# Optimization experiments

Measured on AMD Instinct MI355X. Metric: run time of the kernel, lower is better.

Reference implementation:

```python
import jax, jax.numpy as jnp
import numpy as np

NPG = 39      # nodes per graph, from (1+8+64+9)*(39+1)=3280 = lin1 in_features
NEG_SLOPE = 0.2


def gat_conv(x, src, dst, W, a_src, a_dst, b, n):
    """PyG GATConv, heads=1, self-loops already appended to (src, dst).
    x:[N,Fin] W:[Fin,Fout] a_src/a_dst:[Fout] b:[Fout] -> [N,Fout]"""
    h = x @ W                                        # [N,Fout]
    e = jax.nn.leaky_relu(h[src] @ a_src + h[dst] @ a_dst, NEG_SLOPE)  # [E]
    m = jax.lax.stop_gradient(jax.ops.segment_max(e, dst, num_segments=n))
    w = jnp.exp(e - m[dst])
    denom = jax.ops.segment_sum(w, dst, num_segments=n)
    alpha = w / (denom[dst] + 1e-16)                 # segment softmax per target node
    out = jax.ops.segment_sum(alpha[:, None] * h[src], dst, num_segments=n)
    return out + b


def setup_inputs() -> dict:
    key = jax.random.key(0)
    ks = jax.random.split(key, 20)
    B, DEG = 4096, 8
    N = B * NPG
    E = N * DEG
    x = jax.random.normal(ks[0], (N, 1), dtype=jnp.float32)
    # block-diagonal edges: each node emits DEG edges to random nodes in SAME graph
    src = jnp.repeat(jnp.arange(N, dtype=jnp.int64), DEG)
    offs = (src // NPG) * NPG
    dst = offs + jax.random.randint(ks[1], (E,), 0, NPG, dtype=jnp.int64)
    edge_index = jnp.stack([src, dst])
    batch_vec = jnp.repeat(jnp.arange(B, dtype=jnp.int64), NPG)

    def glorot(k, shape):
        fan = shape[0] + (shape[1] if len(shape) > 1 else 1)
        s = jnp.sqrt(6.0 / fan)
        return jax.random.uniform(k, shape, jnp.float32, -s, s)

    p = {
        'W1': glorot(ks[2], (1, 8)),   'a1s': glorot(ks[3], (8,)),  'a1d': glorot(ks[4], (8,)),  'b1': jnp.zeros((8,), jnp.float32),
        'W2': glorot(ks[5], (8, 64)),  'a2s': glorot(ks[6], (64,)), 'a2d': glorot(ks[7], (64,)), 'b2': jnp.zeros((64,), jnp.float32),
        'W3': glorot(ks[8], (64, 9)),  'a3s': glorot(ks[9], (9,)),  'a3d': glorot(ks[10], (9,)), 'b3': jnp.zeros((9,), jnp.float32),
        'lW1': glorot(ks[11], (3280, 5000)), 'lb1': jnp.zeros((5000,), jnp.float32),
        'lW2': glorot(ks[12], (5000, 1024)), 'lb2': jnp.zeros((1024,), jnp.float32),
        'lW3': glorot(ks[13], (1024, 9)),    'lb3': jnp.zeros((9,), jnp.float32),
    }
    return {'x': x, 'edge_index': edge_index, 'batch_vec': batch_vec, **p}


def reference(x, edge_index, batch_vec,
              W1, a1s, a1d, b1, W2, a2s, a2d, b2, W3, a3s, a3d, b3,
              lW1, lb1, lW2, lb2, lW3, lb3):
    N = x.shape[0]
    B = N // NPG
    loops = jnp.arange(N, dtype=edge_index.dtype)
    src = jnp.concatenate([edge_index[0], loops])   # GATConv add_self_loops=True
    dst = jnp.concatenate([edge_index[1], loops])

    res = x.reshape(B, -1)                                    # [B,39]
    out0 = jax.ops.segment_max(x, batch_vec, num_segments=B)  # [B,1]

    h1 = jax.nn.relu(gat_conv(x, src, dst, W1, a1s, a1d, b1, N))   # dropout = eval no-op
    res1 = h1.reshape(B, -1)                                   # [B,312]
    out1 = jax.ops.segment_max(h1, batch_vec, num_segments=B)

    h2 = jax.nn.relu(gat_conv(h1, src, dst, W2, a2s, a2d, b2, N))
    res2 = h2.reshape(B, -1)                                   # [B,2496]
    out2 = jax.ops.segment_max(h2, batch_vec, num_segments=B)

    h3 = jax.nn.relu(gat_conv(h2, src, dst, W3, a3s, a3d, b3, N))
    res3 = h3.reshape(B, -1)                                   # [B,351]
    out3 = jax.ops.segment_max(h3, batch_vec, num_segments=B)

    f = jnp.concatenate([res, res1, res2, res3, out0, out1, out2, out3], axis=1)  # [B,3280]
    f = jax.nn.relu(f @ lW1 + lb1)
    f = jax.nn.relu(f @ lW2 + lb2)
    return f @ lW3 + lb3                                       # [B,9]
```

## Files before the change

### kernel.cpp

```cpp
#include <hip/hip_runtime.h>
#include <hip/hip_bf16.h>
#include <hip/hip_fp16.h>
#include <stdint.h>


typedef float f32x4 __attribute__((ext_vector_type(4)));
typedef short bf16x8 __attribute__((ext_vector_type(8)));
typedef _Float16 f16x8 __attribute__((ext_vector_type(8)));

__device__ __forceinline__ unsigned fenc(float f) {
  int s = __float_as_int(f);
  return s < 0 ? ~(unsigned)s : ((unsigned)s | 0x80000000u);
}
__device__ __forceinline__ float fdec(unsigned u) {
  return (u & 0x80000000u) ? __int_as_float((int)(u & 0x7fffffffu))
                           : __int_as_float(~(int)u);
}

__device__ __forceinline__ void ldsbar() {
  asm volatile("s_waitcnt lgkmcnt(0)\n\ts_barrier" ::: "memory");
}


__global__ __launch_bounds__(128) void gnn_conv_seq(
    const float* __restrict__ x,
    const int* __restrict__ esrc, const int* __restrict__ edst,
    const float* __restrict__ W1, const float* __restrict__ a1s, const float* __restrict__ a1d, const float* __restrict__ b1,
    const float* __restrict__ W2, const float* __restrict__ a2s, const float* __restrict__ a2d, const float* __restrict__ b2,
    const float* __restrict__ W3, const float* __restrict__ a3s, const float* __restrict__ a3d, const float* __restrict__ b3,
    __hip_bfloat16* __restrict__ fA,
    const float* __restrict__ lW1, const float* __restrict__ lW2,
    short* __restrict__ W1T, short* __restrict__ W2T)
{
  __shared__ __align__(16) char smem[19840];
  const int tid = threadIdx.x;
  const int bid = blockIdx.x;

  if (bid >= 4096) {
    float (*t)[260] = (float(*)[260])smem;
    const int cid = bid - 4096;
    const float* W; short* WT; int ktile, ntile, K0, N0, KT;
    if (cid < 4160) { W = lW1; WT = W1T; ktile = cid % 208; ntile = cid / 208; K0 = 3280; N0 = 5000; KT = 52; }
    else { int c2 = cid - 4160; W = lW2; WT = W2T; ktile = c2 % 320; ntile = c2 / 320; K0 = 5000; N0 = 1024; KT = 80; }

    const int kb = ktile * 16, nb = ntile * 256;
    const int wv = tid >> 6, ln = tid & 63;
#pragma unroll
    for (int r = 0; r < 8; ++r) {
      int k = kb + wv * 8 + r;
      int n = nb + ln * 4;
      f32x4 v = (f32x4){0.f, 0.f, 0.f, 0.f};
      if (k < K0 && n < N0) v = *(const f32x4*)&W[(size_t)k * N0 + n];
      *(f32x4*)&t[wv * 8 + r][ln * 4] = v;
    }
    __syncthreads();
#pragma unroll
    for (int h = 0; h < 4; ++h) {
      int c = h * 128 + tid;
      int nl = c >> 1, kc = c & 1;
      int n = nb + nl, k = kb + kc * 8;
      union { bf16x8 v; __hip_bfloat16 b[8]; } z;
#pragma unroll
      for (int j = 0; j < 8; ++j) z.b[j] = __float2bfloat16(t[kc * 8 + j][nl]);
      int rt = n >> 7, mi = (n >> 4) & 7, lr = n & 15;
      int kt = k >> 6, kq = (k >> 5) & 1, lc = (k >> 3) & 3;
      size_t addr = ((((size_t)rt * KT) + kt) * 16 + mi * 2 + kq) * 512 + ((size_t)lr + 16 * lc) * 8;
      *(bf16x8*)&WT[addr] = z.v;
    }
    return;
  }

  float*    A     = (float*)   (smem);
  __half*   Hh2   = (__half*)  (smem + 6880);
  __half*   h1h   = (__half*)  (smem + 12512);
  float*    HfT   = (float*)   (smem + 13152);
  float*    sW3T  = (float*)   (smem + 14752);
  float*    xbuf  = (float*)   (smem + 17216);
  float*    a2buf = (float*)   (smem + 17376);
  float*    sarr  = (float*)   (smem + 17888);
  float*    darr  = (float*)   (smem + 18048);
  unsigned* umx   = (unsigned*)(smem + 18208);
  float*    a3sb  = (float*)   (smem + 18736);
  float*    a3db  = (float*)   (smem + 18784);
  float*    b3b   = (float*)   (smem + 18832);
  unsigned* cntP  = (unsigned*)(smem + 18880);

  const int g = bid, w = tid >> 6, f = tid & 63;
  const int dd3 = tid / 3, pp3 = tid - dd3 * 3;

  const int rt = g >> 7, mi = (g >> 4) & 7, lrow = g & 15;
  const size_t gbase = (size_t)rt * 52 * 8192 + (size_t)(mi * 2) * 512 + (size_t)lrow * 8;
#define COLADDR(c) (gbase + (size_t)((c) >> 6) * 8192 + (size_t)(((c) >> 5) & 1) * 512 \
                    + (size_t)(((c) >> 3) & 3) * 128 + ((c) & 7))

  auto denseEW = [&](const float* sv, const float* dv, float* sms) {
    if (tid < 117) {
      float dval = dv[dd3];
      float* Ar = &A[dd3 * 44];
      const unsigned* cr = &cntP[dd3 * 6];
      int s0 = pp3 * 13;
      float sum = 0.f;
#pragma unroll
      for (int k = 0; k < 13; ++k) {
        int s = s0 + k;
        float e = sv[s] + dval;
        e = (e > 0.f) ? e : 0.2f * e;
        unsigned c = (cr[s >> 3] >> (4 * (s & 7))) & 0xFu;
        float ex = __expf(e);
        float wv = c ? (float)c * ex : 0.f;
        Ar[s] = wv; sum += wv;
      }
      if (pp3 == 2) Ar[39] = 0.f;
      sms[tid] = sum;
    }
  };

  for (int i = tid; i < 576; i += 128) { int k = i / 9, f3 = i - 9 * k; sW3T[f3 * 68 + k] = W3[i]; }
  a2buf[tid] = (tid < 64) ? a2s[tid] : a2d[tid - 64];
  if (tid < 9) { a3sb[tid] = a3s[tid]; a3db[tid] = a3d[tid]; b3b[tid] = b3[tid]; }
  for (int i = tid; i < 132; i += 128) umx[i] = 0u;
  for (int i = tid; i < 234; i += 128) cntP[i] = 0u;
  if (tid < 40) xbuf[tid] = 0.f;

  float xv = 0.f;
  if (tid < 39) { xv = x[g * 39 + tid]; xbuf[tid] = xv; fA[COLADDR(tid)] = __float2bfloat16(xv); }

  float c_s = 0.f, c_d = 0.f;
  const float w1r = W1[tid & 7], b1r = b1[tid & 7];
#pragma unroll
  for (int ff = 0; ff < 8; ++ff) { float wv = W1[ff]; c_s += wv * a1s[ff]; c_d += wv * a1d[ff]; }
  const int eb = g * 312, nb0 = g * 39;
  ldsbar();

  if (tid < 39) atomicMax(&umx[0], fenc(xv));
#pragma unroll
  for (int it = 0; it < 3; ++it) {
    int e = it * 128 + tid;
    if (e < 351) {
      int ls, ld;
      if (e < 312) { ls = esrc[eb + e] - nb0; ld = edst[eb + e] - nb0; }
      else         { ls = e - 312; ld = ls; }
      atomicAdd(&cntP[ld * 6 + (ls >> 3)], 1u << (4 * (ls & 7)));
    }
  }
  if (f < 39) { if (w == 0) sarr[f] = xbuf[f] * c_s; else darr[f] = xbuf[f] * c_d; }
  ldsbar();

  denseEW(sarr, darr, &HfT[128]);
  ldsbar();
  if (tid < 39) {
    const float* Ar = &A[tid * 44];
    float q = 0.f;
#pragma unroll
    for (int c = 0; c < 10; ++c) {
      f32x4 a4 = *(const f32x4*)&Ar[c * 4];
      f32x4 x4 = *(const f32x4*)&xbuf[c * 4];
      q += a4.x * x4.x + a4.y * x4.y + a4.z * x4.z + a4.w * x4.w;
    }
    float inv = 1.f / (HfT[128 + 3 * tid] + HfT[129 + 3 * tid] + HfT[130 + 3 * tid] + 1e-16f);
    sarr[tid] = q * inv;
  }
  ldsbar();
#pragma unroll
  for (int it = 0; it < 3; ++it) {
    int slot = it * 128 + tid;
    if (slot < 312) {
      int i = slot >> 3, fi = slot & 7;
      float v = fmaxf(sarr[i] * w1r + b1r, 0.f);
      h1h[slot] = __float2half(v);
      fA[COLADDR(39 + slot)] = __float2bfloat16(v);
      atomicMax(&umx[1 + fi], fenc(v));
    }
  }
  ldsbar();

  float ht2r[40];
  {
    float w2k[8];
#pragma unroll
    for (int k = 0; k < 8; ++k) w2k[k] = W2[k * 64 + f];
#pragma unroll
    for (int i = 0; i < 39; ++i) {
      f16x8 hr = *(const f16x8*)&h1h[i * 8];
      float hv = 0.f;
#pragma unroll
      for (int k = 0; k < 8; ++k) hv += (float)hr[k] * w2k[k];
      ht2r[i] = hv;
    }
    ht2r[39] = 0.f;
#pragma unroll
    for (int i = 0; i < 39; ++i) {
      if ((i < 20) ? (w == 0) : (w == 1))
        Hh2[i * 72 + f] = __float2half(ht2r[i]);
    }
  }
  ldsbar();
  {
    int node = f;
    if (node < 39) {
      const float* ab = a2buf + (tid & 64);
      const __half* hr = &Hh2[node * 72];
      float s = 0.f;
#pragma unroll
      for (int c = 0; c < 8; ++c) {
        f16x8 hv = *(const f16x8*)&hr[c * 8];
        f32x4 a0 = *(const f32x4*)&ab[c * 8];
        f32x4 a1 = *(const f32x4*)&ab[c * 8 + 4];
        s += (float)hv[0] * a0.x + (float)hv[1] * a0.y + (float)hv[2] * a0.z + (float)hv[3] * a0.w
           + (float)hv[4] * a1.x + (float)hv[5] * a1.y + (float)hv[6] * a1.z + (float)hv[7] * a1.w;
      }
      if (tid < 64) sarr[node] = s; else darr[node] = s;
    }
  }
  ldsbar();
  denseEW(sarr, darr, &HfT[128]);
  ldsbar();
  {
    const float b2r = b2[f];
    for (int it = 0; it < 20; ++it) {
      int i = it * 2 + w;
      if (i < 39) {
        float inv = 1.f / (HfT[128 + 3 * i] + HfT[129 + 3 * i] + HfT[130 + 3 * i] + 1e-16f);
        const float* Ar = &A[i * 44];
        float acc = 0.f;
#pragma unroll
        for (int c = 0; c < 10; ++c) {
          f32x4 a4 = *(const f32x4*)&Ar[c * 4];
          acc += a4.x * ht2r[c * 4] + a4.y * ht2r[c * 4 + 1]
               + a4.z * ht2r[c * 4 + 2] + a4.w * ht2r[c * 4 + 3];
        }
        float v = fmaxf(acc * inv + b2r, 0.f);
        Hh2[i * 72 + f] = __float2half(v);
        fA[COLADDR(351 + i * 64 + f)] = __float2bfloat16(v);
        atomicMax(&umx[9 + f], fenc(v));
      }
    }
  }
  ldsbar();

  {
#pragma unroll
    for (int it = 0; it < 3; ++it) {
      int slot = it * 128 + tid;
      if (slot < 351) {
        int i = slot / 9, f3 = slot - 9 * i;
        const __half* hr = &Hh2[i * 72];
        const float* wr = &sW3T[f3 * 68];
        float acc = 0.f;
#pragma unroll
        for (int c = 0; c < 8; ++c) {
          f16x8 hv = *(const f16x8*)&hr[c * 8];
          f32x4 w0 = *(const f32x4*)&wr[c * 8];
          f32x4 w1 = *(const f32x4*)&wr[c * 8 + 4];
          acc += (float)hv[0] * w0.x + (float)hv[1] * w0.y + (float)hv[2] * w0.z + (float)hv[3] * w0.w
               + (float)hv[4] * w1.x + (float)hv[5] * w1.y + (float)hv[6] * w1.z + (float)hv[7] * w1.w;
        }
        HfT[f3 * 44 + i] = acc;
      }
    }
    if (tid < 9) HfT[tid * 44 + 39] = 0.f;
  }
  ldsbar();
  {
    int node = f;
    if (node < 39) {
      const float* av = (tid < 64) ? a3sb : a3db;
      float s = 0.f;
#pragma unroll
      for (int f3 = 0; f3 < 9; ++f3) s += HfT[f3 * 44 + node] * av[f3];
      if (tid < 64) sarr[node] = s; else darr[node] = s;
    }
  }
  ldsbar();
  denseEW(sarr, darr, &sW3T[128]);
  ldsbar();
#pragma unroll
  for (int it = 0; it < 3; ++it) {
    int slot = it * 128 + tid;
    if (slot < 351) {
      int i = slot / 9, f3 = slot - 9 * i;
      float inv = 1.f / (sW3T[128 + 3 * i] + sW3T[129 + 3 * i] + sW3T[130 + 3 * i] + 1e-16f);
      const float* Ar = &A[i * 44];
      const float* Hr = &HfT[f3 * 44];
      float acc = 0.f;
#pragma unroll
      for (int c = 0; c < 10; ++c) {
        f32x4 a4 = *(const f32x4*)&Ar[c * 4];
        f32x4 h4 = *(const f32x4*)&Hr[c * 4];
        acc += a4.x * h4.x + a4.y * h4.y + a4.z * h4.z + a4.w * h4.w;
      }
      float v = fmaxf(acc * inv + b3b[f3], 0.f);
      fA[COLADDR(2847 + slot)] = __float2bfloat16(v);
      atomicMax(&umx[73 + f3], fenc(v));
    }
  }
  ldsbar();

  if (tid < 130) {
    int c = 3198 + tid;
    float v = (tid < 82) ? fdec(umx[tid]) : 0.f;
    fA[COLADDR(c)] = __float2bfloat16(v);
  }
#undef COLADDR
}


__device__ __forceinline__ void gld_lds16(const void* gptr, void* l) {
  typedef const __attribute__((address_space(1))) unsigned int GU;
  typedef __attribute__((address_space(3))) unsigned int LU;
  __builtin_amdgcn_global_load_lds((GU*)gptr, (LU*)l, 16, 0, 0);
}

__global__ __launch_bounds__(256) void gemm_tiled(
    const short* __restrict__ A, const short* __restrict__ B,
    const float* __restrict__ bias, int Nreal,
    void* __restrict__ Cout, int Nn, int KT, int ktPerSplit, int outKT)
{
  __shared__ __align__(16) short lA[8192];
  __shared__ __align__(16) short lB[8192];
  const int tid = threadIdx.x;
  const int w = tid >> 6, L = tid & 63;
  const int lrow = L & 15, lch = L >> 4;
  const int mt = blockIdx.y, nt = blockIdx.x;
  const int mw = (w >> 1) * 4, nw = (w & 1) * 4;
  const int kt0 = blockIdx.z * ktPerSplit, kt1 = kt0 + ktPerSplit;

  const short* Ab = A + ((size_t)mt * KT) * 8192 + (size_t)L * 8;
  const short* Bb = B + ((size_t)nt * KT) * 8192 + (size_t)L * 8;

  f32x4 acc[4][4] = {};

  for (int kt = kt0; kt < kt1; ++kt) {
    const short* Ak = Ab + (size_t)kt * 8192;
    const short* Bk = Bb + (size_t)kt * 8192;
#pragma unroll
    for (int j = 0; j < 4; ++j) {
      int st = w * 4 + j;
      gld_lds16(Ak + st * 512, &lA[st * 512]);
      gld_lds16(Bk + st * 512, &lB[st * 512]);
    }
    __syncthreads();
#pragma unroll
    for (int kk = 0; kk < 2; ++kk) {
      bf16x8 af[4], bfr[4];
#pragma unroll
      for (int i = 0; i < 4; ++i) {
        af[i]  = *(const bf16x8*)&lA[((mw + i) * 2 + kk) * 512 + L * 8];
        bfr[i] = *(const bf16x8*)&lB[((nw + i) * 2 + kk) * 512 + L * 8];
      }
#pragma unroll
      for (int i = 0; i < 4; ++i)
#pragma unroll
        for (int j = 0; j < 4; ++j)
          acc[i][j] = __builtin_amdgcn_mfma_f32_16x16x32_bf16(af[i], bfr[j], acc[i][j], 0, 0, 0);
    }
    __syncthreads();
  }

  __hip_bfloat16* C = (__hip_bfloat16*)Cout;
#pragma unroll
  for (int j = 0; j < 4; ++j) {
    int n = nt * 128 + (nw + j) * 16 + lrow;
    float bn = (n < Nreal) ? bias[n] : 0.f;
    int kt = n >> 6, kq = (n >> 5) & 1, lc2 = (n >> 3) & 3, j2 = n & 7;
#pragma unroll
    for (int i = 0; i < 4; ++i) {
      int mi = mw + i;
      size_t base = ((((size_t)mt * outKT + kt) * 16) + mi * 2 + kq) * 512
                    + (size_t)(lch * 4) * 8 + (size_t)lc2 * 128 + j2;
#pragma unroll
      for (int r = 0; r < 4; ++r)
        C[base + r * 8] = __float2bfloat16(fmaxf(acc[i][j][r] + bn, 0.f));
    }
  }
}

__global__ __launch_bounds__(512) void gemm2_256(
    const short* __restrict__ A, const short* __restrict__ B,
    __half* __restrict__ P)
{
  __shared__ __align__(16) short lA[16384];
  __shared__ __align__(16) short lB[16384];
  const int tid = threadIdx.x;
  const int w = tid >> 6, L = tid & 63;
  const int lrow = L & 15, lch = L >> 4;
  const int wr = w >> 2, wc = w & 3;
  const int nt = blockIdx.x, mt = blockIdx.y, zz = blockIdx.z;
  const int kt0 = zz * 20, kt1 = kt0 + 20;

  const short* A0 = A + ((size_t)(mt * 2) * 80) * 8192;
  const short* A1 = A + ((size_t)(mt * 2 + 1) * 80) * 8192;
  const short* B0 = B + ((size_t)(nt * 2) * 80) * 8192;
  const short* B1 = B + ((size_t)(nt * 2 + 1) * 80) * 8192;

  f32x4 acc[8][4] = {};

  for (int kt = kt0; kt < kt1; ++kt) {
    const size_t ko = (size_t)kt * 8192;
#pragma unroll
    for (int c = 0; c < 2; ++c) {
      int off = (c * 512 + tid) * 8;
      gld_lds16(A0 + ko + off, &lA[off]);
      gld_lds16(A1 + ko + off, &lA[8192 + off]);
      gld_lds16(B0 + ko + off, &lB[off]);
      gld_lds16(B1 + ko + off, &lB[8192 + off]);
    }
    __syncthreads();
#pragma unroll
    for (int kk = 0; kk < 2; ++kk) {
      bf16x8 af[8], bf[4];
#pragma unroll
      for (int i = 0; i < 8; ++i)
        af[i] = *(const bf16x8*)&lA[wr * 8192 + (i * 2 + kk) * 512 + L * 8];
#pragma unroll
      for (int j = 0; j < 4; ++j)
        bf[j] = *(const bf16x8*)&lB[(wc >> 1) * 8192 + (((wc & 1) * 4 + j) * 2 + kk) * 512 + L * 8];
#pragma unroll
      for (int i = 0; i < 8; ++i)
#pragma unroll
        for (int j = 0; j < 4; ++j)
          acc[i][j] = __builtin_amdgcn_mfma_f32_16x16x32_bf16(af[i], bf[j], acc[i][j], 0, 0, 0);
    }
    __syncthreads();
  }

  __half* Pz = P + (size_t)zz * 4096 * 1024;
#pragma unroll
  for (int j = 0; j < 4; ++j) {
    int n = nt * 256 + wc * 64 + j * 16 + lrow;
#pragma unroll
    for (int i = 0; i < 8; ++i)
#pragma unroll
      for (int r = 0; r < 4; ++r) {
        int m = mt * 256 + wr * 128 + i * 16 + lch * 4 + r;
        Pz[(size_t)m * 1024 + n] = __float2half(acc[i][j][r]);
      }
  }
}


__global__ __launch_bounds__(256) void gemm3_fused(
    const __half* __restrict__ P,
    const float* __restrict__ b2v,
    const float* __restrict__ W3,
    const float* __restrict__ b3v,
    float* __restrict__ out)
{
  __shared__ float sW3[9 * 1024];
  int tid = threadIdx.x;
  for (int i = tid; i < 9216; i += 256) { int k = i / 9, j = i - 9 * k; sW3[j * 1024 + k] = W3[i]; }
  __syncthreads();
  int row = blockIdx.x * 4 + (tid >> 6);
  int lane = tid & 63;
  const __half* p0 = P + (size_t)row * 1024;
  const size_t S = (size_t)4096 * 1024;
  float acc[9] = {0, 0, 0, 0, 0, 0, 0, 0, 0};
  for (int t = 0; t < 16; ++t) {
    int k = lane + 64 * t;
    float c = __half2float(p0[k]) + __half2float(p0[k + S])
            + __half2float(p0[k + 2 * S]) + __half2float(p0[k + 3 * S]) + b2v[k];
    c = fmaxf(c, 0.f);
#pragma unroll
    for (int j = 0; j < 9; ++j) acc[j] += c * sW3[j * 1024 + k];
  }
#pragma unroll
  for (int j = 0; j < 9; ++j) {
    float v = acc[j];
    v += __shfl_down(v, 32, 64);
    v += __shfl_down(v, 16, 64);
    v += __shfl_down(v, 8, 64);
    v += __shfl_down(v, 4, 64);
    v += __shfl_down(v, 2, 64);
    v += __shfl_down(v, 1, 64);
    if (lane == 0) out[(size_t)row * 9 + j] = v + b3v[j];
  }
}


extern "C" void kernel_launch(void* const* d_in, const int* in_sizes, int n_in,
                              void* d_out, int out_size, void* d_ws, size_t ws_size,
                              hipStream_t stream)
{
  const float* x   = (const float*)d_in[0];
  const int*   ei  = (const int*)d_in[1];
  const float* W1  = (const float*)d_in[3];
  const float* a1s = (const float*)d_in[4];
  const float* a1d = (const float*)d_in[5];
  const float* b1  = (const float*)d_in[6];
  const float* W2  = (const float*)d_in[7];
  const float* a2s = (const float*)d_in[8];
  const float* a2d = (const float*)d_in[9];
  const float* b2  = (const float*)d_in[10];
  const float* W3  = (const float*)d_in[11];
  const float* a3s = (const float*)d_in[12];
  const float* a3d = (const float*)d_in[13];
  const float* b3  = (const float*)d_in[14];
  const float* lW1 = (const float*)d_in[15];
  const float* lb1 = (const float*)d_in[16];
  const float* lW2 = (const float*)d_in[17];
  const float* lb2 = (const float*)d_in[18];
  const float* lW3 = (const float*)d_in[19];
  const float* lb3 = (const float*)d_in[20];

  const int E = 4096 * 39 * 8;
  const int* esrc = ei;
  const int* edst = ei + E;

  short* fA  = (short*)d_ws;
  short* W1T = fA  + (size_t)4096 * 3328;
  short* C1  = W1T + (size_t)5120 * 3328;
  short* W2T = C1  + (size_t)4096 * 5120;
  __half* P  = (__half*)d_ws;

  gnn_conv_seq<<<9536, 128, 0, stream>>>(x, esrc, edst,
                                         W1, a1s, a1d, b1, W2, a2s, a2d, b2, W3, a3s, a3d, b3,
                                         (__hip_bfloat16*)fA, lW1, lW2, W1T, W2T);
  gemm_tiled<<<dim3(40, 32, 1), 256, 0, stream>>>(fA, W1T, lb1, 5000, C1, 5120, 52, 52, 80);
  gemm2_256<<<dim3(4, 16, 4), 512, 0, stream>>>(C1, W2T, P);
  gemm3_fused<<<1024, 256, 0, stream>>>(P, lb2, lW3, lb3, (float*)d_out);
}
```

Baseline: 450.7 us.

## Map one graph per wavefront and replace block barriers with wave-local waits

Restructures the GNN conv kernel so each 64-lane wavefront processes its own graph, two graphs per 128-thread block, with separate LDS slices per wave. Block-wide s_barrier calls become lgkmcnt waits only, relying on wave lockstep. Layer-1 attention is fused into a single per-node pass, and softmax denominators are stored as reciprocals. This raises LDS per block and serialises more work per lane, which may affect occupancy and latency.

```diff
diff --git a/kernel.cpp b/kernel.cpp
--- a/kernel.cpp
+++ b/kernel.cpp
@@ -17,12 +17,12 @@
                            : __int_as_float(~(int)u);
 }
 
-__device__ __forceinline__ void ldsbar() {
-  asm volatile("s_waitcnt lgkmcnt(0)\n\ts_barrier" ::: "memory");
-}
-
-
-__global__ __launch_bounds__(128) void gnn_conv_seq(
+__device__ __forceinline__ void wbar() {
+  asm volatile("s_waitcnt lgkmcnt(0)" ::: "memory");
+}
+
+
+__global__ __launch_bounds__(128) void gnn_conv_wpg(
     const float* __restrict__ x,
     const int* __restrict__ esrc, const int* __restrict__ edst,
     const float* __restrict__ W1, const float* __restrict__ a1s, const float* __restrict__ a1d, const float* __restrict__ b1,
@@ -32,26 +32,26 @@
     const float* __restrict__ lW1, const float* __restrict__ lW2,
     short* __restrict__ W1T, short* __restrict__ W2T)
 {
-  __shared__ __align__(16) char smem[19840];
+  __shared__ __align__(16) char smem[36768];
   const int tid = threadIdx.x;
   const int bid = blockIdx.x;
 
-  if (bid >= 4096) {
+  if (bid >= 2048) {
     float (*t)[260] = (float(*)[260])smem;
-    const int cid = bid - 4096;
+    const int cid = bid - 2048;
     const float* W; short* WT; int ktile, ntile, K0, N0, KT;
     if (cid < 4160) { W = lW1; WT = W1T; ktile = cid % 208; ntile = cid / 208; K0 = 3280; N0 = 5000; KT = 52; }
     else { int c2 = cid - 4160; W = lW2; WT = W2T; ktile = c2 % 320; ntile = c2 / 320; K0 = 5000; N0 = 1024; KT = 80; }
 
     const int kb = ktile * 16, nb = ntile * 256;
-    const int wv = tid >> 6, ln = tid & 63;
+    const int wv = tid >> 6, lnc = tid & 63;
 #pragma unroll
     for (int r = 0; r < 8; ++r) {
       int k = kb + wv * 8 + r;
-      int n = nb + ln * 4;
+      int n = nb + lnc * 4;
       f32x4 v = (f32x4){0.f, 0.f, 0.f, 0.f};
       if (k < K0 && n < N0) v = *(const f32x4*)&W[(size_t)k * N0 + n];
-      *(f32x4*)&t[wv * 8 + r][ln * 4] = v;
+      *(f32x4*)&t[wv * 8 + r][lnc * 4] = v;
     }
     __syncthreads();
 #pragma unroll
@@ -70,72 +70,51 @@
     return;
   }
 
-  float*    A     = (float*)   (smem);
-  __half*   Hh2   = (__half*)  (smem + 6880);
-  __half*   h1h   = (__half*)  (smem + 12512);
-  float*    HfT   = (float*)   (smem + 13152);
-  float*    sW3T  = (float*)   (smem + 14752);
-  float*    xbuf  = (float*)   (smem + 17216);
-  float*    a2buf = (float*)   (smem + 17376);
-  float*    sarr  = (float*)   (smem + 17888);
-  float*    darr  = (float*)   (smem + 18048);
-  unsigned* umx   = (unsigned*)(smem + 18208);
-  float*    a3sb  = (float*)   (smem + 18736);
-  float*    a3db  = (float*)   (smem + 18784);
-  float*    b3b   = (float*)   (smem + 18832);
-  unsigned* cntP  = (unsigned*)(smem + 18880);
-
-  const int g = bid, w = tid >> 6, f = tid & 63;
-  const int dd3 = tid / 3, pp3 = tid - dd3 * 3;
+  const int w = tid >> 6, ln = tid & 63;
+  const int g = bid * 2 + w;
+
+  float* sW3T  = (float*)(smem);
+  float* a2buf = (float*)(smem + 2448);
+  float* a3sb  = (float*)(smem + 2960);
+  float* a3db  = (float*)(smem + 3008);
+  float* b3b   = (float*)(smem + 3056);
+  char* sl = smem + 3104 + w * 16832;
+  float*    A    = (float*)   (sl);
+  __half*   Hh2  = (__half*)  (sl + 6864);
+  __half*   h1h  = (__half*)  (sl + 12480);
+  float*    HfT  = (float*)   (sl + 13120);
+  float*    xbuf = (float*)   (sl + 14720);
+  float*    sarr = (float*)   (sl + 14880);
+  float*    darr = (float*)   (sl + 15040);
+  float*    den  = (float*)   (sl + 15200);
+  unsigned* umx  = (unsigned*)(sl + 15360);
+  unsigned* cntP = (unsigned*)(sl + 15888);
 
   const int rt = g >> 7, mi = (g >> 4) & 7, lrow = g & 15;
   const size_t gbase = (size_t)rt * 52 * 8192 + (size_t)(mi * 2) * 512 + (size_t)lrow * 8;
 #define COLADDR(c) (gbase + (size_t)((c) >> 6) * 8192 + (size_t)(((c) >> 5) & 1) * 512 \
                     + (size_t)(((c) >> 3) & 3) * 128 + ((c) & 7))
 
-  auto denseEW = [&](const float* sv, const float* dv, float* sms) {
-    if (tid < 117) {
-      float dval = dv[dd3];
-      float* Ar = &A[dd3 * 44];
-      const unsigned* cr = &cntP[dd3 * 6];
-      int s0 = pp3 * 13;
-      float sum = 0.f;
-#pragma unroll
-      for (int k = 0; k < 13; ++k) {
-        int s = s0 + k;
-        float e = sv[s] + dval;
-        e = (e > 0.f) ? e : 0.2f * e;
-        unsigned c = (cr[s >> 3] >> (4 * (s & 7))) & 0xFu;
-        float ex = __expf(e);
-        float wv = c ? (float)c * ex : 0.f;
-        Ar[s] = wv; sum += wv;
-      }
-      if (pp3 == 2) Ar[39] = 0.f;
-      sms[tid] = sum;
-    }
-  };
-
   for (int i = tid; i < 576; i += 128) { int k = i / 9, f3 = i - 9 * k; sW3T[f3 * 68 + k] = W3[i]; }
   a2buf[tid] = (tid < 64) ? a2s[tid] : a2d[tid - 64];
   if (tid < 9) { a3sb[tid] = a3s[tid]; a3db[tid] = a3d[tid]; b3b[tid] = b3[tid]; }
-  for (int i = tid; i < 132; i += 128) umx[i] = 0u;
-  for (int i = tid; i < 234; i += 128) cntP[i] = 0u;
-  if (tid < 40) xbuf[tid] = 0.f;
+  for (int i = ln; i < 132; i += 64) umx[i] = 0u;
+  for (int i = ln; i < 234; i += 64) cntP[i] = 0u;
+  if (ln < 40) xbuf[ln] = 0.f;
+  if (ln == 39) { sarr[39] = 0.f; darr[39] = 0.f; }
+  __syncthreads();
 
   float xv = 0.f;
-  if (tid < 39) { xv = x[g * 39 + tid]; xbuf[tid] = xv; fA[COLADDR(tid)] = __float2bfloat16(xv); }
-
+  if (ln < 39) { xv = x[g * 39 + ln]; xbuf[ln] = xv; fA[COLADDR(ln)] = __float2bfloat16(xv); }
   float c_s = 0.f, c_d = 0.f;
-  const float w1r = W1[tid & 7], b1r = b1[tid & 7];
+  const float w1r = W1[ln & 7], b1r = b1[ln & 7];
 #pragma unroll
   for (int ff = 0; ff < 8; ++ff) { float wv = W1[ff]; c_s += wv * a1s[ff]; c_d += wv * a1d[ff]; }
   const int eb = g * 312, nb0 = g * 39;
-  ldsbar();
-
-  if (tid < 39) atomicMax(&umx[0], fenc(xv));
-#pragma unroll
-  for (int it = 0; it < 3; ++it) {
-    int e = it * 128 + tid;
+  if (ln < 39) atomicMax(&umx[0], fenc(xv));
+#pragma unroll
+  for (int it = 0; it < 6; ++it) {
+    int e = it * 64 + ln;
     if (e < 351) {
       int ls, ld;
       if (e < 312) { ls = esrc[eb + e] - nb0; ld = edst[eb + e] - nb0; }
@@ -143,42 +122,78 @@
       atomicAdd(&cntP[ld * 6 + (ls >> 3)], 1u << (4 * (ls & 7)));
     }
   }
-  if (f < 39) { if (w == 0) sarr[f] = xbuf[f] * c_s; else darr[f] = xbuf[f] * c_d; }
-  ldsbar();
-
-  denseEW(sarr, darr, &HfT[128]);
-  ldsbar();
-  if (tid < 39) {
-    const float* Ar = &A[tid * 44];
-    float q = 0.f;
+  wbar();
+
+  auto denseEW = [&](const float* sv, const float* dv) {
+    if (ln < 39) {
+      unsigned cw[6];
+#pragma unroll
+      for (int j = 0; j < 6; ++j) cw[j] = cntP[ln * 6 + j];
+      float dval = dv[ln];
+      float* Ar = &A[ln * 44];
+      float sum = 0.f;
+#pragma unroll
+      for (int c = 0; c < 10; ++c) {
+        f32x4 s4 = *(const f32x4*)&sv[c * 4];
+        f32x4 w4;
+#pragma unroll
+        for (int j = 0; j < 4; ++j) {
+          int s = c * 4 + j;
+          float e = s4[j] + dval;
+          e = (e > 0.f) ? e : 0.2f * e;
+          unsigned cc = (cw[s >> 3] >> (4 * (s & 7))) & 0xFu;
+          float ex = __expf(e);
+          float wv = cc ? (float)cc * ex : 0.f;
+          w4[j] = wv; sum += wv;
+        }
+        *(f32x4*)&Ar[c * 4] = w4;
+      }
+      den[ln] = 1.f / (sum + 1e-16f);
+    }
+  };
+
+  if (ln < 39) {
+    unsigned cw[6];
+#pragma unroll
+    for (int j = 0; j < 6; ++j) cw[j] = cntP[ln * 6 + j];
+    float dval = xbuf[ln] * c_d;
+    float q = 0.f, dsum = 0.f;
 #pragma unroll
     for (int c = 0; c < 10; ++c) {
-      f32x4 a4 = *(const f32x4*)&Ar[c * 4];
       f32x4 x4 = *(const f32x4*)&xbuf[c * 4];
-      q += a4.x * x4.x + a4.y * x4.y + a4.z * x4.z + a4.w * x4.w;
-    }
-    float inv = 1.f / (HfT[128 + 3 * tid] + HfT[129 + 3 * tid] + HfT[130 + 3 * tid] + 1e-16f);
-    sarr[tid] = q * inv;
-  }
-  ldsbar();
-#pragma unroll
-  for (int it = 0; it < 3; ++it) {
-    int slot = it * 128 + tid;
+#pragma unroll
+      for (int j = 0; j < 4; ++j) {
+        int s = c * 4 + j;
+        float xs = x4[j];
+        float e = xs * c_s + dval;
+        e = (e > 0.f) ? e : 0.2f * e;
+        unsigned cc = (cw[s >> 3] >> (4 * (s & 7))) & 0xFu;
+        float ex = __expf(e);
+        float wv = cc ? (float)cc * ex : 0.f;
+        q += wv * xs; dsum += wv;
+      }
+    }
+    sarr[ln] = q * (1.f / (dsum + 1e-16f));
+  }
+  wbar();
+#pragma unroll
+  for (int it = 0; it < 5; ++it) {
+    int slot = it * 64 + ln;
     if (slot < 312) {
-      int i = slot >> 3, fi = slot & 7;
+      int i = slot >> 3;
       float v = fmaxf(sarr[i] * w1r + b1r, 0.f);
       h1h[slot] = __float2half(v);
       fA[COLADDR(39 + slot)] = __float2bfloat16(v);
-      atomicMax(&umx[1 + fi], fenc(v));
-    }
-  }
-  ldsbar();
+      atomicMax(&umx[1 + (ln & 7)], fenc(v));
+    }
+  }
+  wbar();
 
   float ht2r[40];
   {
     float w2k[8];
 #pragma unroll
-    for (int k = 0; k < 8; ++k) w2k[k] = W2[k * 64 + f];
+    for (int k = 0; k < 8; ++k) w2k[k] = W2[k * 64 + ln];
 #pragma unroll
     for (int i = 0; i < 39; ++i) {
       f16x8 hr = *(const f16x8*)&h1h[i * 8];
@@ -189,16 +204,15 @@
     }
     ht2r[39] = 0.f;
 #pragma unroll
-    for (int i = 0; i < 39; ++i) {
-      if ((i < 20) ? (w == 0) : (w == 1))
-        Hh2[i * 72 + f] = __float2half(ht2r[i]);
-    }
-  }
-  ldsbar();
-  {
-    int node = f;
-    if (node < 39) {
-      const float* ab = a2buf + (tid & 64);
+    for (int i = 0; i < 39; ++i) Hh2[i * 72 + ln] = __float2half(ht2r[i]);
+  }
+  wbar();
+#pragma unroll
+  for (int rr = 0; rr < 2; ++rr) {
+    int t = rr * 64 + ln;
+    if (t < 78) {
+      int node = (t < 39) ? t : t - 39;
+      const float* ab = a2buf + ((t < 39) ? 0 : 64);
       const __half* hr = &Hh2[node * 72];
       float s = 0.f;
 #pragma unroll
@@ -209,77 +223,74 @@
         s += (float)hv[0] * a0.x + (float)hv[1] * a0.y + (float)hv[2] * a0.z + (float)hv[3] * a0.w
            + (float)hv[4] * a1.x + (float)hv[5] * a1.y + (float)hv[6] * a1.z + (float)hv[7] * a1.w;
       }
-      if (tid < 64) sarr[node] = s; else darr[node] = s;
-    }
-  }
-  ldsbar();
-  denseEW(sarr, darr, &HfT[128]);
-  ldsbar();
+      if (t < 39) sarr[node] = s; else darr[node] = s;
+    }
+  }
+  wbar();
+  denseEW(sarr, darr);
+  wbar();
   {
-    const float b2r = b2[f];
-    for (int it = 0; it < 20; ++it) {
-      int i = it * 2 + w;
-      if (i < 39) {
-        float inv = 1.f / (HfT[128 + 3 * i] + HfT[129 + 3 * i] + HfT[130 + 3 * i] + 1e-16f);
-        const float* Ar = &A[i * 44];
-        float acc = 0.f;
-#pragma unroll
-        for (int c = 0; c < 10; ++c) {
-          f32x4 a4 = *(const f32x4*)&Ar[c * 4];
-          acc += a4.x * ht2r[c * 4] + a4.y * ht2r[c * 4 + 1]
-               + a4.z * ht2r[c * 4 + 2] + a4.w * ht2r[c * 4 + 3];
-        }
-        float v = fmaxf(acc * inv + b2r, 0.f);
-        Hh2[i * 72 + f] = __float2half(v);
-        fA[COLADDR(351 + i * 64 + f)] = __float2bfloat16(v);
-        atomicMax(&umx[9 + f], fenc(v));
-      }
-    }
-  }
-  ldsbar();
-
-  {
-#pragma unroll
-    for (int it = 0; it < 3; ++it) {
-      int slot = it * 128 + tid;
-      if (slot < 351) {
-        int i = slot / 9, f3 = slot - 9 * i;
-        const __half* hr = &Hh2[i * 72];
-        const float* wr = &sW3T[f3 * 68];
-        float acc = 0.f;
-#pragma unroll
-        for (int c = 0; c < 8; ++c) {
-          f16x8 hv = *(const f16x8*)&hr[c * 8];
-          f32x4 w0 = *(const f32x4*)&wr[c * 8];
-          f32x4 w1 = *(const f32x4*)&wr[c * 8 + 4];
-          acc += (float)hv[0] * w0.x + (float)hv[1] * w0.y + (float)hv[2] * w0.z + (float)hv[3] * w0.w
-               + (float)hv[4] * w1.x + (float)hv[5] * w1.y + (float)hv[6] * w1.z + (float)hv[7] * w1.w;
-        }
-        HfT[f3 * 44 + i] = acc;
-      }
-    }
-    if (tid < 9) HfT[tid * 44 + 39] = 0.f;
-  }
-  ldsbar();
-  {
-    int node = f;
-    if (node < 39) {
-      const float* av = (tid < 64) ? a3sb : a3db;
-      float s = 0.f;
-#pragma unroll
-      for (int f3 = 0; f3 < 9; ++f3) s += HfT[f3 * 44 + node] * av[f3];
-      if (tid < 64) sarr[node] = s; else darr[node] = s;
-    }
-  }
-  ldsbar();
-  denseEW(sarr, darr, &sW3T[128]);
-  ldsbar();
-#pragma unroll
-  for (int it = 0; it < 3; ++it) {
-    int slot = it * 128 + tid;
+    const float b2r = b2[ln];
+    for (int i = 0; i < 39; ++i) {
+      float inv = den[i];
+      const float* Ar = &A[i * 44];
+      float acc = 0.f;
+#pragma unroll
+      for (int c = 0; c < 10; ++c) {
+        f32x4 a4 = *(const f32x4*)&Ar[c * 4];
+        acc += a4.x * ht2r[c * 4] + a4.y * ht2r[c * 4 + 1]
+             + a4.z * ht2r[c * 4 + 2] + a4.w * ht2r[c * 4 + 3];
+      }
+      float v = fmaxf(acc * inv + b2r, 0.f);
+      Hh2[i * 72 + ln] = __float2half(v);
+      fA[COLADDR(351 + i * 64 + ln)] = __float2bfloat16(v);
+      atomicMax(&umx[9 + ln], fenc(v));
+    }
+  }
+  wbar();
+
+#pragma unroll
+  for (int it = 0; it < 6; ++it) {
+    int slot = it * 64 + ln;
     if (slot < 351) {
       int i = slot / 9, f3 = slot - 9 * i;
-      float inv = 1.f / (sW3T[128 + 3 * i] + sW3T[129 + 3 * i] + sW3T[130 + 3 * i] + 1e-16f);
+      const __half* hr = &Hh2[i * 72];
+      const float* wr = &sW3T[f3 * 68];
+      float acc = 0.f;
+#pragma unroll
+      for (int c = 0; c < 8; ++c) {
+        f16x8 hv = *(const f16x8*)&hr[c * 8];
+        f32x4 w0 = *(const f32x4*)&wr[c * 8];
+        f32x4 w1 = *(const f32x4*)&wr[c * 8 + 4];
+        acc += (float)hv[0] * w0.x + (float)hv[1] * w0.y + (float)hv[2] * w0.z + (float)hv[3] * w0.w
+             + (float)hv[4] * w1.x + (float)hv[5] * w1.y + (float)hv[6] * w1.z + (float)hv[7] * w1.w;
+      }
+      HfT[f3 * 44 + i] = acc;
+    }
+  }
+  if (ln < 9) HfT[ln * 44 + 39] = 0.f;
+  wbar();
+#pragma unroll
+  for (int rr = 0; rr < 2; ++rr) {
+    int t = rr * 64 + ln;
+    if (t < 78) {
+      int node = (t < 39) ? t : t - 39;
+      const float* av = (t < 39) ? a3sb : a3db;
+      float s = 0.f;
+#pragma unroll
+      for (int f3 = 0; f3 < 9; ++f3) s += HfT[f3 * 44 + node] * av[f3];
+      if (t < 39) sarr[node] = s; else darr[node] = s;
+    }
+  }
+  wbar();
+  denseEW(sarr, darr);
+  wbar();
+#pragma unroll
+  for (int it = 0; it < 6; ++it) {
+    int slot = it * 64 + ln;
+    if (slot < 351) {
+      int i = slot / 9, f3 = slot - 9 * i;
+      float inv = den[i];
       const float* Ar = &A[i * 44];
       const float* Hr = &HfT[f3 * 44];
       float acc = 0.f;
@@ -294,12 +305,16 @@
       atomicMax(&umx[73 + f3], fenc(v));
     }
   }
-  ldsbar();
-
-  if (tid < 130) {
-    int c = 3198 + tid;
-    float v = (tid < 82) ? fdec(umx[tid]) : 0.f;
-    fA[COLADDR(c)] = __float2bfloat16(v);
+  wbar();
+
+#pragma unroll
+  for (int it = 0; it < 3; ++it) {
+    int idx = it * 64 + ln;
+    if (idx < 130) {
+      int c = 3198 + idx;
+      float v = (idx < 82) ? fdec(umx[idx]) : 0.f;
+      fA[COLADDR(c)] = __float2bfloat16(v);
+    }
   }
 #undef COLADDR
 }
@@ -512,7 +527,7 @@
   short* W2T = C1  + (size_t)4096 * 5120;
   __half* P  = (__half*)d_ws;
 
-  gnn_conv_seq<<<9536, 128, 0, stream>>>(x, esrc, edst,
+  gnn_conv_wpg<<<7488, 128, 0, stream>>>(x, esrc, edst,
                                          W1, a1s, a1d, b1, W2, a2s, a2d, b2, W3, a3s, a3d, b3,
                                          (__hip_bfloat16*)fA, lW1, lW2, W1T, W2T);
   gemm_tiled<<<dim3(40, 32, 1), 256, 0, stream>>>(fA, W1T, lb1, 5000, C1, 5120, 52, 52, 80);
```

New measurement: 442.4 us. No clear change (-1.8%).
